# Kernel optimization log

Measured on AMD Instinct MI355X. Metric: run time of the kernel, lower is better.

## Reference

```python
import jax, jax.numpy as jnp
import numpy as np

B, C, S, D = 16, 32, 64, 512
DFF, E = 2048, 8


def setup_inputs() -> dict:
    key = jax.random.key(0)
    ks = jax.random.split(key, 16)
    std = 0.02
    return {
        'x': jax.random.normal(ks[0], (B, C, S, D), jnp.float32),
        'baseline': jax.random.normal(ks[1], (B, C, S, D), jnp.float32),
        'attnres': jax.random.normal(ks[2], (B, C, S, D), jnp.float32),
        'shared_w1': jax.random.normal(ks[3], (DFF, D), jnp.float32) * std,
        'shared_b1': jnp.zeros((DFF,), jnp.float32),
        'shared_w2': jax.random.normal(ks[4], (D, DFF), jnp.float32) * std,
        'shared_b2': jnp.zeros((D,), jnp.float32),
        'spa_router_w': jax.random.normal(ks[5], (E, 3 * D), jnp.float32) * std,
        'spa_router_b': jnp.zeros((E,), jnp.float32),
        'spe_router_w': jax.random.normal(ks[6], (E, 3 * D), jnp.float32) * std,
        'spe_router_b': jnp.zeros((E,), jnp.float32),
        'spa_w1': jax.random.normal(ks[7], (E, DFF, D), jnp.float32) * std,
        'spa_b1': jnp.zeros((E, DFF), jnp.float32),
        'spa_w2': jax.random.normal(ks[8], (E, D, DFF), jnp.float32) * std,
        'spa_b2': jnp.zeros((E, D), jnp.float32),
        'spe_w1': jax.random.normal(ks[9], (E, DFF, D), jnp.float32) * std,
        'spe_b1': jnp.zeros((E, DFF), jnp.float32),
        'spe_w2': jax.random.normal(ks[10], (E, D, DFF), jnp.float32) * std,
        'spe_b2': jnp.zeros((E, D), jnp.float32),
    }


def _route(feat, rw, rb):
    # feat [B, 3D] -> top-1 expert index [B] and its softmax gate weight [B]
    logits = feat @ rw.T + rb            # [B, E]
    p = jax.nn.softmax(logits, axis=-1)
    idx = jnp.argmax(logits, axis=-1)    # [B]
    w = jnp.take_along_axis(p, idx[:, None], axis=-1)[:, 0]
    return idx, w


def _specialist(xf, idx, w1, b1, w2, b2):
    # xf [B, T, D]; per-sample gather of expert weights then batched FFN
    W1, B1 = w1[idx], b1[idx]            # [B, DFF, D], [B, DFF]
    W2, B2 = w2[idx], b2[idx]            # [B, D, DFF], [B, D]
    h = jax.nn.gelu(jnp.einsum('btd,bfd->btf', xf, W1) + B1[:, None, :])
    return jnp.einsum('btf,bdf->btd', h, W2) + B2[:, None, :]


def reference(x, baseline, attnres, shared_w1, shared_b1, shared_w2, shared_b2,
              spa_router_w, spa_router_b, spe_router_w, spe_router_b,
              spa_w1, spa_b1, spa_w2, spa_b2, spe_w1, spe_b1, spe_w2, spe_b2):
    b, d = x.shape[0], x.shape[-1]
    xf = x.reshape(b, -1, d)  # [B, T, D]
    # sample-level AttnRes router features: [B, 3*d_model]
    feat = jnp.concatenate([
        baseline.mean(axis=(1, 2)),
        attnres.mean(axis=(1, 2)),
        (attnres - baseline).mean(axis=(1, 2)),
    ], axis=-1)
    spa_idx, spa_w = _route(feat, spa_router_w, spa_router_b)
    spe_idx, spe_w = _route(feat, spe_router_w, spe_router_b)
    # shared dense FFN (dropout=0 eval)
    shared = jax.nn.gelu(xf @ shared_w1.T + shared_b1) @ shared_w2.T + shared_b2
    spa_out = _specialist(xf, spa_idx, spa_w1, spa_b1, spa_w2, spa_b2)
    spe_out = _specialist(xf, spe_idx, spe_w1, spe_b1, spe_w2, spe_b2)
    y = shared + spa_w[:, None, None] * spa_out + spe_w[:, None, None] * spe_out
    return y.reshape(x.shape)
```

## Files before the change

### kernel.cpp

```cpp
#include <hip/hip_runtime.h>
#include <cstdint>
#include <cstddef>

#define DEV __device__ __forceinline__

typedef unsigned short u16;
typedef _Float16 f16x8 __attribute__((ext_vector_type(8)));
typedef float f32x4 __attribute__((ext_vector_type(4)));

static constexpr int NB  = 16;
static constexpr int T   = 2048;
static constexpr int D   = 512;
static constexpr int DFF = 2048;
static constexpr int NE  = 8;
static constexpr int FEAT = 3 * D;

#define MFMA16 __builtin_amdgcn_mfma_f32_16x16x32_f16

DEV u16 f2h(float f) {
  _Float16 h = (_Float16)f;
  union { _Float16 h; u16 u; } cv; cv.h = h; return cv.u;
}

DEV float gelu_fast(float x) {
  const float t = x * x;
  const float p = x * fmaf(t, -0.07135481627f, -1.59576912161f);
  return __fdividef(x, 1.0f + __expf(p));
}


__global__ void k_part(const float* __restrict__ base, const float* __restrict__ attn,
                       float* __restrict__ part) {
  const int b = blockIdx.x >> 4, ch = blockIdx.x & 15;
  const int d = threadIdx.x;
  const size_t o = ((size_t)b * T + (size_t)ch * 128) * D + d;
  const float* pb = base + o;
  const float* pa = attn + o;
  float sb = 0.f, sa = 0.f;
  for (int r = 0; r < 128; ++r) { sb += pb[(size_t)r * D]; sa += pa[(size_t)r * D]; }
  part[(b * 16 + ch) * D + d] = sb;
  part[NB * 16 * D + (b * 16 + ch) * D + d] = sa;
}

__global__ void k_feat(const float* __restrict__ part, float* __restrict__ feat) {
  const int b = blockIdx.x, d = threadIdx.x;
  float sb = 0.f, sa = 0.f;
  for (int ch = 0; ch < 16; ++ch) {
    sb += part[(b * 16 + ch) * D + d];
    sa += part[NB * 16 * D + (b * 16 + ch) * D + d];
  }
  sb *= (1.0f / 2048.0f); sa *= (1.0f / 2048.0f);
  feat[b * FEAT + d] = sb;
  feat[b * FEAT + D + d] = sa;
  feat[b * FEAT + 2 * D + d] = sa - sb;
}

__global__ void k_zero(int* __restrict__ used) {
  used[threadIdx.x] = 0;
}

__global__ void k_route(const float* __restrict__ feat,
                        const float* __restrict__ rw0, const float* __restrict__ rb0,
                        const float* __restrict__ rw1, const float* __restrict__ rb1,
                        int* __restrict__ idx, float* __restrict__ gate,
                        int* __restrict__ used) {
  const int r = blockIdx.x >> 4, b = blockIdx.x & 15;
  const float* rw = (r == 0) ? rw0 : rw1;
  const float* rb = (r == 0) ? rb0 : rb1;
  const int l = threadIdx.x;
  float p[8];
#pragma unroll
  for (int e = 0; e < 8; ++e) p[e] = 0.f;
  const float* f = feat + b * FEAT;
  for (int k = l; k < FEAT; k += 64) {
    const float fv = f[k];
#pragma unroll
    for (int e = 0; e < 8; ++e) p[e] += fv * rw[e * FEAT + k];
  }
#pragma unroll
  for (int off = 32; off >= 1; off >>= 1) {
#pragma unroll
    for (int e = 0; e < 8; ++e) p[e] += __shfl_xor(p[e], off);
  }
  if (l == 0) {
    float best = -1e30f; int bi = 0;
    float lg[8];
#pragma unroll
    for (int e = 0; e < 8; ++e) {
      lg[e] = p[e] + rb[e];
      if (lg[e] > best) { best = lg[e]; bi = e; }
    }
    float s = 0.f;
#pragma unroll
    for (int e = 0; e < 8; ++e) s += expf(lg[e] - best);
    idx[r * 16 + b] = bi;
    gate[r * 16 + b] = 1.0f / s;
    atomicOr(&used[r * 8 + bi], 1);
  }
}

__global__ void k_btot(const float* __restrict__ b2s, const float* __restrict__ b2a,
                       const float* __restrict__ b2e, const int* __restrict__ idx,
                       const float* __restrict__ gate, float* __restrict__ btot) {
  const int b = blockIdx.x, d = threadIdx.x;
  const int ia = idx[b], ie = idx[16 + b];
  const float ga = gate[b], ge = gate[16 + b];
  btot[b * D + d] = b2s[d] + ga * b2a[ia * D + d] + ge * b2e[ie * D + d];
}

__global__ void k_cast(const float* __restrict__ s, u16* __restrict__ d, long n) {
  const long i = ((long)blockIdx.x * blockDim.x + threadIdx.x) * 4;
  if (i >= n) return;
  const float4 v = *(const float4*)(s + i);
  const unsigned int lo = (unsigned int)f2h(v.x) | ((unsigned int)f2h(v.y) << 16);
  const unsigned int hi = (unsigned int)f2h(v.z) | ((unsigned int)f2h(v.w) << 16);
  *(uint2*)(d + i) = make_uint2(lo, hi);
}

__global__ void k_cast_gated(const float* __restrict__ s, u16* __restrict__ d,
                             const int* __restrict__ used) {
  const int e = blockIdx.x >> 10;
  if (!used[e]) return;
  const long i = (long)e * (DFF * D) + ((long)(blockIdx.x & 1023) * 256 + threadIdx.x) * 4;
  const float4 v = *(const float4*)(s + i);
  const unsigned int lo = (unsigned int)f2h(v.x) | ((unsigned int)f2h(v.y) << 16);
  const unsigned int hi = (unsigned int)f2h(v.z) | ((unsigned int)f2h(v.w) << 16);
  *(uint2*)(d + i) = make_uint2(lo, hi);
}


DEV void ld_lds16(const void* g, void* l) {
  __builtin_amdgcn_global_load_lds((const __attribute__((address_space(1))) void*)g,
                                   (__attribute__((address_space(3))) void*)l, 16, 0, 0);
}

#define BAR __builtin_amdgcn_s_barrier()
#define LGKM0 do { asm volatile("s_waitcnt lgkmcnt(0)" ::: "memory"); \
                   __builtin_amdgcn_sched_barrier(0); } while (0)
#define VMW2 asm volatile("s_waitcnt vmcnt(2)" ::: "memory")
#define VMW0 asm volatile("s_waitcnt vmcnt(0)" ::: "memory")

#define STG_A(tt, h, sb) do { const long ko_ = (long)(tt) * 64;                          \
    ld_lds16(((h) ? gA10 : gA00) + ko_, (char*)As + (sb) * 32768 + (h) * 16384 + dR0);   \
    ld_lds16(((h) ? gA11 : gA01) + ko_, (char*)As + (sb) * 32768 + (h) * 16384 + dR1); } while (0)
#define STG_B(tt, h, sb) do { const long ko_ = (long)(tt) * 64;                          \
    ld_lds16(((h) ? gB10 : gB00) + ko_, (char*)Bs + (sb) * 32768 + (h) * 16384 + dR0);   \
    ld_lds16(((h) ? gB11 : gB01) + ko_, (char*)Bs + (sb) * 32768 + (h) * 16384 + dR1); } while (0)

#define RD_A(dst, mb, sb) do {                                                           \
    _Pragma("unroll") for (int m_ = 0; m_ < 4; ++m_)                                     \
      _Pragma("unroll") for (int k_ = 0; k_ < 2; ++k_)                                   \
        dst[m_][k_] = *(const f16x8*)((const char*)As + (sb) * 32768 + avb[k_] +         \
                                      ((mb) + m_) * 2048); } while (0)
#define RD_B(dst, nb, sb) do {                                                           \
    _Pragma("unroll") for (int n_ = 0; n_ < 2; ++n_)                                     \
      _Pragma("unroll") for (int k_ = 0; k_ < 2; ++k_)                                   \
        dst[n_][k_] = *(const f16x8*)((const char*)Bs + (sb) * 32768 + bvb[k_] +         \
                                      ((nb) + n_) * 2048); } while (0)

#define QUAD(av, bv, mb, nb) do { __builtin_amdgcn_s_setprio(1);                         \
    _Pragma("unroll") for (int m_ = 0; m_ < 4; ++m_)                                     \
      _Pragma("unroll") for (int n_ = 0; n_ < 2; ++n_) {                                 \
        acc[(mb)+m_][(nb)+n_] = MFMA16(av[m_][0], bv[n_][0], acc[(mb)+m_][(nb)+n_],0,0,0); \
        acc[(mb)+m_][(nb)+n_] = MFMA16(av[m_][1], bv[n_][1], acc[(mb)+m_][(nb)+n_],0,0,0); \
      }                                                                                  \
    __builtin_amdgcn_s_setprio(0); } while (0)

#define TILE(tt, sb, STGN, STGA0, VMN) do {                                              \
    RD_A(avLO, 0, sb); RD_B(bvA, 0, sb);                                                 \
    if (STGN) { STG_A((tt)+1, 1, (sb)^1); STG_B((tt)+1, 0, (sb)^1); STG_B((tt)+1, 1, (sb)^1); } \
    BAR; LGKM0; QUAD(avLO, bvA, 0, 0); BAR;                                              \
    RD_B(bvB, 2, sb);                                                                    \
    BAR; LGKM0; QUAD(avLO, bvB, 0, 2); BAR;                                              \
    RD_A(avHI, 4, sb);                                                                   \
    BAR; LGKM0; QUAD(avHI, bvB, 4, 2); BAR;                                              \
    if (STGA0) STG_A((tt)+2, 0, sb);                                                     \
    BAR; __builtin_amdgcn_sched_barrier(0); QUAD(avHI, bvA, 4, 0);                       \
    if ((VMN) == 2) VMW2; else if ((VMN) == 0) VMW0;                                     \
    BAR;                                                                                 \
  } while (0)

template <int NT>
DEV void gemm_8p(const u16* __restrict__ A, int lda, const u16* __restrict__ B, int ldb,
                 u16* As, u16* Bs, f32x4 (&acc)[8][4]) {
  static_assert(NT >= 8 && (NT % 2) == 0, "NT even, >= 8");
  const int tid = threadIdx.x;
  const int lane = tid & 63, wid = tid >> 6;
  const int wr = wid >> 2, wc = wid & 3;

  const int srow = lane >> 3;
  const int scol = (lane & 7) ^ srow;
  const int rj0 = wid * 16 + srow;
  const int rj1 = rj0 + 8;
  const u16* gA00 = A + (size_t)(  0 + rj0) * lda + scol * 8;
  const u16* gA01 = A + (size_t)(  0 + rj1) * lda + scol * 8;
  const u16* gA10 = A + (size_t)(128 + rj0) * lda + scol * 8;
  const u16* gA11 = A + (size_t)(128 + rj1) * lda + scol * 8;
  const u16* gB00 = B + (size_t)(  0 + rj0) * ldb + scol * 8;
  const u16* gB01 = B + (size_t)(  0 + rj1) * ldb + scol * 8;
  const u16* gB10 = B + (size_t)(128 + rj0) * ldb + scol * 8;
  const u16* gB11 = B + (size_t)(128 + rj1) * ldb + scol * 8;
  const int dR0 = (wid * 16) * 128;
  const int dR1 = dR0 + 1024;

  const int aR = wr * 128 + (lane & 15);
  const int bR = wc * 64 + (lane & 15);
  const int sH = lane >> 4;
  int avb[2], bvb[2];
#pragma unroll
  for (int k_ = 0; k_ < 2; ++k_) {
    const int s_ = (k_ * 4 + sH);
    avb[k_] = aR * 128 + ((s_ ^ (lane & 7)) * 16);
    bvb[k_] = bR * 128 + ((s_ ^ (lane & 7)) * 16);
  }

  f16x8 avLO[4][2], avHI[4][2], bvA[2][2], bvB[2][2];

  STG_A(0, 0, 0); STG_A(0, 1, 0); STG_B(0, 0, 0); STG_B(0, 1, 0);
  STG_A(1, 0, 1);
  VMW2; BAR;

  for (int tp = 0; tp < (NT - 2) / 2; ++tp) {
    TILE(2 * tp,     0, true, true, 2);
    TILE(2 * tp + 1, 1, true, true, 2);
  }
  TILE(NT - 2, 0, true,  false, 0);
  TILE(NT - 1, 1, false, false, -1);
}

template <int BANK>
__global__ __launch_bounds__(512) void k_ffn1(
    const u16* __restrict__ xh, const u16* __restrict__ w1, const float* __restrict__ b1,
    const int* __restrict__ idx, const float* __restrict__ gate, u16* __restrict__ h) {
  __shared__ alignas(16) u16 As[2 * 16384];
  __shared__ alignas(16) u16 Bs[2 * 16384];
  int wg = blockIdx.x;
  const int q = (int)gridDim.x >> 3;
  wg = (wg & 7) * q + (wg >> 3);
  const int b  = wg >> 6;
  const int mt = (wg >> 3) & 7;
  const int nt = wg & 7;

  const int e   = (BANK == 0) ? 0 : idx[(BANK - 1) * 16 + b];
  const float g = (BANK == 0) ? 1.0f : gate[(BANK - 1) * 16 + b];
  const u16* Ab = xh + ((size_t)b * T + (size_t)mt * 256) * D;
  const u16* Bb = w1 + (size_t)e * DFF * D + (size_t)nt * 256 * D;
  const float* bb = b1 + (size_t)e * DFF;

  f32x4 acc[8][4];
#pragma unroll
  for (int m = 0; m < 8; ++m)
#pragma unroll
    for (int n = 0; n < 4; ++n)
#pragma unroll
      for (int r = 0; r < 4; ++r) acc[m][n][r] = 0.f;

  gemm_8p<8>(Ab, D, Bb, D, As, Bs, acc);

  const int lane = threadIdx.x & 63, wid = threadIdx.x >> 6;
  const int wr = wid >> 2, wc = wid & 3;
  const int rr = (lane >> 4) << 2, cc = lane & 15;
  const int mrow = mt * 256 + wr * 128;
  const int ncol = nt * 256 + wc * 64;
  u16* hb = h + (size_t)b * T * DFF;
  u16* wsl = (u16*)As + wid * (16 * 72);
  const int rdrow = lane >> 2;
  const int rdcb  = (lane & 3) * 2;
  float bias[4];
#pragma unroll
  for (int n = 0; n < 4; ++n) bias[n] = bb[ncol + n * 16 + cc];
#pragma unroll
  for (int m = 0; m < 8; ++m) {
#pragma unroll
    for (int n = 0; n < 4; ++n) {
      const f32x4 a = acc[m][n];
#pragma unroll
      for (int r = 0; r < 4; ++r)
        wsl[(rr + r) * 72 + n * 16 + cc] = f2h(gelu_fast(a[r] + bias[n]) * g);
    }
    asm volatile("s_waitcnt lgkmcnt(0)" ::: "memory");
    __builtin_amdgcn_sched_barrier(0);
    const uint4 v0 = *(const uint4*)(wsl + rdrow * 72 + rdcb * 8);
    const uint4 v1 = *(const uint4*)(wsl + rdrow * 72 + rdcb * 8 + 8);
    u16* dst = hb + (size_t)(mrow + m * 16 + rdrow) * DFF + ncol + rdcb * 8;
    *(uint4*)dst = v0;
    *(uint4*)(dst + 8) = v1;
    asm volatile("s_waitcnt lgkmcnt(0)" ::: "memory");
    __builtin_amdgcn_sched_barrier(0);
  }
}

template <int BANK>
__global__ __launch_bounds__(512) void k_ffn2(
    const u16* __restrict__ h, const u16* __restrict__ w2, const float* __restrict__ btot,
    const int* __restrict__ idx, float* __restrict__ out) {
  __shared__ alignas(16) u16 As[2 * 16384];
  __shared__ alignas(16) u16 Bs[2 * 16384];
  int wg = blockIdx.x;
  const int q = (int)gridDim.x >> 3;
  wg = (wg & 7) * q + (wg >> 3);
  const int b  = wg >> 4;
  const int mt = (wg >> 1) & 7;
  const int nt = wg & 1;

  const int e = (BANK == 0) ? 0 : idx[(BANK - 1) * 16 + b];
  const u16* Ab = h + ((size_t)b * T + (size_t)mt * 256) * DFF;
  const u16* Bb = w2 + (size_t)e * D * DFF + (size_t)nt * 256 * DFF;

  f32x4 acc[8][4];
#pragma unroll
  for (int m = 0; m < 8; ++m)
#pragma unroll
    for (int n = 0; n < 4; ++n)
#pragma unroll
      for (int r = 0; r < 4; ++r) acc[m][n][r] = 0.f;

  gemm_8p<32>(Ab, DFF, Bb, DFF, As, Bs, acc);

  const int lane = threadIdx.x & 63, wid = threadIdx.x >> 6;
  const int wr = wid >> 2, wc = wid & 3;
  const int rr = (lane >> 4) << 2, cc = lane & 15;
  const int mrow = mt * 256 + wr * 128;
  const int ncol = nt * 256 + wc * 64;
  float* ob = out + (size_t)b * T * D;
  float* wsl = (float*)(void*)As + wid * (16 * 68);
  float btv[4];
#pragma unroll
  for (int n = 0; n < 4; ++n)
    btv[n] = (BANK == 0) ? btot[b * D + ncol + n * 16 + cc] : 0.f;
#pragma unroll
  for (int m = 0; m < 8; ++m) {
#pragma unroll
    for (int n = 0; n < 4; ++n) {
      const f32x4 a = acc[m][n];
#pragma unroll
      for (int r = 0; r < 4; ++r)
        wsl[(rr + r) * 68 + n * 16 + cc] = a[r] + btv[n];
    }
    asm volatile("s_waitcnt lgkmcnt(0)" ::: "memory");
    __builtin_amdgcn_sched_barrier(0);
#pragma unroll
    for (int j = 0; j < 4; ++j) {
      const int row = j * 4 + (lane >> 4);
      const int colb = lane & 15;
      f32x4 v = *(const f32x4*)(wsl + row * 68 + colb * 4);
      float* dst = ob + (size_t)(mrow + m * 16 + row) * D + ncol + colb * 4;
      if (BANK != 0) { const f32x4 o = *(const f32x4*)dst; v += o; }
      *(f32x4*)dst = v;
    }
    asm volatile("s_waitcnt lgkmcnt(0)" ::: "memory");
    __builtin_amdgcn_sched_barrier(0);
  }
}


extern "C" void kernel_launch(void* const* d_in, const int* in_sizes, int n_in,
                              void* d_out, int out_size, void* d_ws, size_t ws_size,
                              hipStream_t stream) {
  (void)in_sizes; (void)n_in; (void)out_size; (void)ws_size;
  const float* x    = (const float*)d_in[0];
  const float* base = (const float*)d_in[1];
  const float* attn = (const float*)d_in[2];
  const float* sw1  = (const float*)d_in[3];
  const float* sb1  = (const float*)d_in[4];
  const float* sw2  = (const float*)d_in[5];
  const float* sb2  = (const float*)d_in[6];
  const float* arw  = (const float*)d_in[7];
  const float* arb  = (const float*)d_in[8];
  const float* erw  = (const float*)d_in[9];
  const float* erb  = (const float*)d_in[10];
  const float* aw1  = (const float*)d_in[11];
  const float* ab1  = (const float*)d_in[12];
  const float* aw2  = (const float*)d_in[13];
  const float* ab2  = (const float*)d_in[14];
  const float* ew1  = (const float*)d_in[15];
  const float* eb1  = (const float*)d_in[16];
  const float* ew2  = (const float*)d_in[17];
  const float* eb2  = (const float*)d_in[18];
  float* out = (float*)d_out;

  char* w = (char*)d_ws;
  u16* xh   = (u16*)w;  w += (size_t)NB * T * D * 2;
  u16* hbuf = (u16*)w;  w += (size_t)NB * T * DFF * 2;
  u16* w1s  = (u16*)w;  w += (size_t)DFF * D * 2;
  u16* w2s  = (u16*)w;  w += (size_t)D * DFF * 2;
  u16* w1a  = (u16*)w;  w += (size_t)NE * DFF * D * 2;
  u16* w2a  = (u16*)w;  w += (size_t)NE * D * DFF * 2;
  u16* w1e  = (u16*)w;  w += (size_t)NE * DFF * D * 2;
  u16* w2e  = (u16*)w;  w += (size_t)NE * D * DFF * 2;
  float* part = (float*)w; w += (size_t)2 * NB * 16 * D * 4;
  float* feat = (float*)w; w += (size_t)NB * FEAT * 4;
  int*   idx  = (int*)w;   w += 32 * 4;
  float* gate = (float*)w; w += 32 * 4;
  float* btot = (float*)w; w += (size_t)NB * D * 4;
  int*   used = (int*)w;   w += 16 * 4;

  k_zero<<<dim3(1), dim3(16), 0, stream>>>(used);
  k_part<<<dim3(256), dim3(512), 0, stream>>>(base, attn, part);
  k_feat<<<dim3(16), dim3(512), 0, stream>>>(part, feat);
  k_route<<<dim3(32), dim3(64), 0, stream>>>(feat, arw, arb, erw, erb, idx, gate, used);
  k_btot<<<dim3(16), dim3(512), 0, stream>>>(sb2, ab2, eb2, idx, gate, btot);

  {
    long n;
    n = (long)NB * T * D;  k_cast<<<(unsigned)(n / 1024), 256, 0, stream>>>(x,   xh,  n);
    n = (long)DFF * D;     k_cast<<<(unsigned)(n / 1024), 256, 0, stream>>>(sw1, w1s, n);
    n = (long)D * DFF;     k_cast<<<(unsigned)(n / 1024), 256, 0, stream>>>(sw2, w2s, n);
    k_cast_gated<<<dim3(8192), 256, 0, stream>>>(aw1, w1a, used);
    k_cast_gated<<<dim3(8192), 256, 0, stream>>>(aw2, w2a, used);
    k_cast_gated<<<dim3(8192), 256, 0, stream>>>(ew1, w1e, used + 8);
    k_cast_gated<<<dim3(8192), 256, 0, stream>>>(ew2, w2e, used + 8);
  }

  const dim3 g1(1024), g2(256), blk(512);
  k_ffn1<0><<<g1, blk, 0, stream>>>(xh, w1s, sb1, idx, gate, hbuf);
  k_ffn2<0><<<g2, blk, 0, stream>>>(hbuf, w2s, btot, idx, out);
  k_ffn1<1><<<g1, blk, 0, stream>>>(xh, w1a, ab1, idx, gate, hbuf);
  k_ffn2<1><<<g2, blk, 0, stream>>>(hbuf, w2a, btot, idx, out);
  k_ffn1<2><<<g1, blk, 0, stream>>>(xh, w1e, eb1, idx, gate, hbuf);
  k_ffn2<2><<<g2, blk, 0, stream>>>(hbuf, w2e, btot, idx, out);
}
```

Measured before the change: 719.1 us.

## Make FFN1 blocks persistent over four M tiles and merge cast launches

The first FFN GEMM now launches 256 workgroups instead of 1024. Each workgroup walks four consecutive 256-row M tiles as one continuous 32-step K pipeline and runs the GELU epilogue for each finished tile while loads for the next tile are already in flight. A separate LDS scratch buffer is added for the epilogue so it does not clash with the staging buffers. The seven cast launches are merged into two kernels to cut launch overhead. The trade-offs are extra LDS use and fewer workgroups per GPU, which may lower occupancy and load balance.

```diff
diff --git a/kernel.cpp b/kernel.cpp
--- a/kernel.cpp
+++ b/kernel.cpp
@@ -108,24 +108,37 @@
   btot[b * D + d] = b2s[d] + ga * b2a[ia * D + d] + ge * b2e[ie * D + d];
 }
 
-__global__ void k_cast(const float* __restrict__ s, u16* __restrict__ d, long n) {
-  const long i = ((long)blockIdx.x * blockDim.x + threadIdx.x) * 4;
-  if (i >= n) return;
+
+DEV void cast4(const float* __restrict__ s, u16* __restrict__ d, long i) {
   const float4 v = *(const float4*)(s + i);
   const unsigned int lo = (unsigned int)f2h(v.x) | ((unsigned int)f2h(v.y) << 16);
   const unsigned int hi = (unsigned int)f2h(v.z) | ((unsigned int)f2h(v.w) << 16);
   *(uint2*)(d + i) = make_uint2(lo, hi);
 }
 
-__global__ void k_cast_gated(const float* __restrict__ s, u16* __restrict__ d,
-                             const int* __restrict__ used) {
-  const int e = blockIdx.x >> 10;
-  if (!used[e]) return;
+__global__ void k_cast3(const float* __restrict__ x, const float* __restrict__ sw1,
+                        const float* __restrict__ sw2, u16* __restrict__ xh,
+                        u16* __restrict__ w1s, u16* __restrict__ w2s) {
+  const long NX = (long)NB * T * D;
+  const long NW = (long)DFF * D;
+  const long t = ((long)blockIdx.x * 256 + threadIdx.x) * 4;
+  if (t < NX)               cast4(x,   xh,  t);
+  else if (t < NX + NW)     cast4(sw1, w1s, t - NX);
+  else                      cast4(sw2, w2s, t - NX - NW);
+}
+
+__global__ void k_castg(const float* __restrict__ aw1, const float* __restrict__ aw2,
+                        const float* __restrict__ ew1, const float* __restrict__ ew2,
+                        u16* __restrict__ w1a, u16* __restrict__ w2a,
+                        u16* __restrict__ w1e, u16* __restrict__ w2e,
+                        const int* __restrict__ used) {
+  const int rg = blockIdx.x >> 13;
+  const int e  = (blockIdx.x >> 10) & 7;
+  if (!used[(rg >= 2 ? 8 : 0) + e]) return;
   const long i = (long)e * (DFF * D) + ((long)(blockIdx.x & 1023) * 256 + threadIdx.x) * 4;
-  const float4 v = *(const float4*)(s + i);
-  const unsigned int lo = (unsigned int)f2h(v.x) | ((unsigned int)f2h(v.y) << 16);
-  const unsigned int hi = (unsigned int)f2h(v.z) | ((unsigned int)f2h(v.w) << 16);
-  *(uint2*)(d + i) = make_uint2(lo, hi);
+  const float* s = (rg == 0) ? aw1 : (rg == 1) ? aw2 : (rg == 2) ? ew1 : ew2;
+  u16*         d = (rg == 0) ? w1a : (rg == 1) ? w2a : (rg == 2) ? w1e : w2e;
+  cast4(s, d, i);
 }
 
 
@@ -139,13 +152,6 @@
                    __builtin_amdgcn_sched_barrier(0); } while (0)
 #define VMW2 asm volatile("s_waitcnt vmcnt(2)" ::: "memory")
 #define VMW0 asm volatile("s_waitcnt vmcnt(0)" ::: "memory")
-
-#define STG_A(tt, h, sb) do { const long ko_ = (long)(tt) * 64;                          \
-    ld_lds16(((h) ? gA10 : gA00) + ko_, (char*)As + (sb) * 32768 + (h) * 16384 + dR0);   \
-    ld_lds16(((h) ? gA11 : gA01) + ko_, (char*)As + (sb) * 32768 + (h) * 16384 + dR1); } while (0)
-#define STG_B(tt, h, sb) do { const long ko_ = (long)(tt) * 64;                          \
-    ld_lds16(((h) ? gB10 : gB00) + ko_, (char*)Bs + (sb) * 32768 + (h) * 16384 + dR0);   \
-    ld_lds16(((h) ? gB11 : gB01) + ko_, (char*)Bs + (sb) * 32768 + (h) * 16384 + dR1); } while (0)
 
 #define RD_A(dst, mb, sb) do {                                                           \
     _Pragma("unroll") for (int m_ = 0; m_ < 4; ++m_)                                     \
@@ -165,6 +171,39 @@
         acc[(mb)+m_][(nb)+n_] = MFMA16(av[m_][1], bv[n_][1], acc[(mb)+m_][(nb)+n_],0,0,0); \
       }                                                                                  \
     __builtin_amdgcn_s_setprio(0); } while (0)
+
+#define CORE_SETUP(Abase, Bbase, lda, ldb)                                               \
+  const int srow = lane >> 3;                                                            \
+  const int scol = (lane & 7) ^ srow;                                                    \
+  const int rj0 = wid * 16 + srow;                                                       \
+  const int rj1 = rj0 + 8;                                                               \
+  const u16* gA00 = (Abase) + (size_t)(  0 + rj0) * (lda) + scol * 8;                    \
+  const u16* gA01 = (Abase) + (size_t)(  0 + rj1) * (lda) + scol * 8;                    \
+  const u16* gA10 = (Abase) + (size_t)(128 + rj0) * (lda) + scol * 8;                    \
+  const u16* gA11 = (Abase) + (size_t)(128 + rj1) * (lda) + scol * 8;                    \
+  const u16* gB00 = (Bbase) + (size_t)(  0 + rj0) * (ldb) + scol * 8;                    \
+  const u16* gB01 = (Bbase) + (size_t)(  0 + rj1) * (ldb) + scol * 8;                    \
+  const u16* gB10 = (Bbase) + (size_t)(128 + rj0) * (ldb) + scol * 8;                    \
+  const u16* gB11 = (Bbase) + (size_t)(128 + rj1) * (ldb) + scol * 8;                    \
+  const int dR0 = (wid * 16) * 128;                                                      \
+  const int dR1 = dR0 + 1024;                                                            \
+  const int aR = wr * 128 + (lane & 15);                                                 \
+  const int bR = wc * 64 + (lane & 15);                                                  \
+  const int sH = lane >> 4;                                                              \
+  int avb[2], bvb[2];                                                                    \
+  _Pragma("unroll") for (int k_ = 0; k_ < 2; ++k_) {                                     \
+    const int s_ = (k_ * 4 + sH);                                                        \
+    avb[k_] = aR * 128 + ((s_ ^ (lane & 7)) * 16);                                       \
+    bvb[k_] = bR * 128 + ((s_ ^ (lane & 7)) * 16);                                       \
+  }
+
+
+#define STG_A(tt, h, sb) do { const long ko_ = (long)(tt) * 64;                          \
+    ld_lds16(((h) ? gA10 : gA00) + ko_, (char*)As + (sb) * 32768 + (h) * 16384 + dR0);   \
+    ld_lds16(((h) ? gA11 : gA01) + ko_, (char*)As + (sb) * 32768 + (h) * 16384 + dR1); } while (0)
+#define STG_B(tt, h, sb) do { const long ko_ = (long)(tt) * 64;                          \
+    ld_lds16(((h) ? gB10 : gB00) + ko_, (char*)Bs + (sb) * 32768 + (h) * 16384 + dR0);   \
+    ld_lds16(((h) ? gB11 : gB01) + ko_, (char*)Bs + (sb) * 32768 + (h) * 16384 + dR1); } while (0)
 
 #define TILE(tt, sb, STGN, STGA0, VMN) do {                                              \
     RD_A(avLO, 0, sb); RD_B(bvA, 0, sb);                                                 \
@@ -180,53 +219,28 @@
     BAR;                                                                                 \
   } while (0)
 
-template <int NT>
-DEV void gemm_8p(const u16* __restrict__ A, int lda, const u16* __restrict__ B, int ldb,
-                 u16* As, u16* Bs, f32x4 (&acc)[8][4]) {
-  static_assert(NT >= 8 && (NT % 2) == 0, "NT even, >= 8");
-  const int tid = threadIdx.x;
-  const int lane = tid & 63, wid = tid >> 6;
-  const int wr = wid >> 2, wc = wid & 3;
-
-  const int srow = lane >> 3;
-  const int scol = (lane & 7) ^ srow;
-  const int rj0 = wid * 16 + srow;
-  const int rj1 = rj0 + 8;
-  const u16* gA00 = A + (size_t)(  0 + rj0) * lda + scol * 8;
-  const u16* gA01 = A + (size_t)(  0 + rj1) * lda + scol * 8;
-  const u16* gA10 = A + (size_t)(128 + rj0) * lda + scol * 8;
-  const u16* gA11 = A + (size_t)(128 + rj1) * lda + scol * 8;
-  const u16* gB00 = B + (size_t)(  0 + rj0) * ldb + scol * 8;
-  const u16* gB01 = B + (size_t)(  0 + rj1) * ldb + scol * 8;
-  const u16* gB10 = B + (size_t)(128 + rj0) * ldb + scol * 8;
-  const u16* gB11 = B + (size_t)(128 + rj1) * ldb + scol * 8;
-  const int dR0 = (wid * 16) * 128;
-  const int dR1 = dR0 + 1024;
-
-  const int aR = wr * 128 + (lane & 15);
-  const int bR = wc * 64 + (lane & 15);
-  const int sH = lane >> 4;
-  int avb[2], bvb[2];
-#pragma unroll
-  for (int k_ = 0; k_ < 2; ++k_) {
-    const int s_ = (k_ * 4 + sH);
-    avb[k_] = aR * 128 + ((s_ ^ (lane & 7)) * 16);
-    bvb[k_] = bR * 128 + ((s_ ^ (lane & 7)) * 16);
-  }
-
-  f16x8 avLO[4][2], avHI[4][2], bvA[2][2], bvB[2][2];
-
-  STG_A(0, 0, 0); STG_A(0, 1, 0); STG_B(0, 0, 0); STG_B(0, 1, 0);
-  STG_A(1, 0, 1);
-  VMW2; BAR;
-
-  for (int tp = 0; tp < (NT - 2) / 2; ++tp) {
-    TILE(2 * tp,     0, true, true, 2);
-    TILE(2 * tp + 1, 1, true, true, 2);
-  }
-  TILE(NT - 2, 0, true,  false, 0);
-  TILE(NT - 1, 1, false, false, -1);
-}
+
+#define STG_A1(tt, h, sb) do {                                                           \
+    const long o_ = (long)((tt) >> 3) * (256L * D) + (long)((tt) & 7) * 64;              \
+    ld_lds16(((h) ? gA10 : gA00) + o_, (char*)As + (sb) * 32768 + (h) * 16384 + dR0);    \
+    ld_lds16(((h) ? gA11 : gA01) + o_, (char*)As + (sb) * 32768 + (h) * 16384 + dR1); } while (0)
+#define STG_B1(tt, h, sb) do { const long o_ = (long)((tt) & 7) * 64;                    \
+    ld_lds16(((h) ? gB10 : gB00) + o_, (char*)Bs + (sb) * 32768 + (h) * 16384 + dR0);    \
+    ld_lds16(((h) ? gB11 : gB01) + o_, (char*)Bs + (sb) * 32768 + (h) * 16384 + dR1); } while (0)
+
+#define TILE1(tt, sb, STGN, STGA0, VMN) do {                                             \
+    RD_A(avLO, 0, sb); RD_B(bvA, 0, sb);                                                 \
+    if (STGN) { STG_A1((tt)+1, 1, (sb)^1); STG_B1((tt)+1, 0, (sb)^1); STG_B1((tt)+1, 1, (sb)^1); } \
+    BAR; LGKM0; QUAD(avLO, bvA, 0, 0); BAR;                                              \
+    RD_B(bvB, 2, sb);                                                                    \
+    BAR; LGKM0; QUAD(avLO, bvB, 0, 2); BAR;                                              \
+    RD_A(avHI, 4, sb);                                                                   \
+    BAR; LGKM0; QUAD(avHI, bvB, 4, 2); BAR;                                              \
+    if (STGA0) STG_A1((tt)+2, 0, sb);                                                    \
+    BAR; __builtin_amdgcn_sched_barrier(0); QUAD(avHI, bvA, 4, 0);                       \
+    if ((VMN) == 2) VMW2; else if ((VMN) == 0) VMW0;                                     \
+    BAR;                                                                                 \
+  } while (0)
 
 template <int BANK>
 __global__ __launch_bounds__(512) void k_ffn1(
@@ -234,19 +248,25 @@
     const int* __restrict__ idx, const float* __restrict__ gate, u16* __restrict__ h) {
   __shared__ alignas(16) u16 As[2 * 16384];
   __shared__ alignas(16) u16 Bs[2 * 16384];
+  __shared__ alignas(16) u16 eps[8 * 16 * 72];
   int wg = blockIdx.x;
   const int q = (int)gridDim.x >> 3;
   wg = (wg & 7) * q + (wg >> 3);
-  const int b  = wg >> 6;
-  const int mt = (wg >> 3) & 7;
-  const int nt = wg & 7;
+  const int b   = wg >> 4;
+  const int nt  = (wg >> 1) & 7;
+  const int mtg = wg & 1;
 
   const int e   = (BANK == 0) ? 0 : idx[(BANK - 1) * 16 + b];
   const float g = (BANK == 0) ? 1.0f : gate[(BANK - 1) * 16 + b];
-  const u16* Ab = xh + ((size_t)b * T + (size_t)mt * 256) * D;
+  const u16* Ab = xh + ((size_t)b * T + (size_t)mtg * 1024) * D;
   const u16* Bb = w1 + (size_t)e * DFF * D + (size_t)nt * 256 * D;
   const float* bb = b1 + (size_t)e * DFF;
 
+  const int tid = threadIdx.x;
+  const int lane = tid & 63, wid = tid >> 6;
+  const int wr = wid >> 2, wc = wid & 3;
+  CORE_SETUP(Ab, Bb, D, D)
+
   f32x4 acc[8][4];
 #pragma unroll
   for (int m = 0; m < 8; ++m)
@@ -255,39 +275,56 @@
 #pragma unroll
       for (int r = 0; r < 4; ++r) acc[m][n][r] = 0.f;
 
-  gemm_8p<8>(Ab, D, Bb, D, As, Bs, acc);
-
-  const int lane = threadIdx.x & 63, wid = threadIdx.x >> 6;
-  const int wr = wid >> 2, wc = wid & 3;
-  const int rr = (lane >> 4) << 2, cc = lane & 15;
-  const int mrow = mt * 256 + wr * 128;
+  f16x8 avLO[4][2], avHI[4][2], bvA[2][2], bvB[2][2];
+
+  const int rrE = (lane >> 4) << 2, ccE = lane & 15;
   const int ncol = nt * 256 + wc * 64;
   u16* hb = h + (size_t)b * T * DFF;
-  u16* wsl = (u16*)As + wid * (16 * 72);
+  u16* wslE = eps + wid * (16 * 72);
   const int rdrow = lane >> 2;
   const int rdcb  = (lane & 3) * 2;
   float bias[4];
 #pragma unroll
-  for (int n = 0; n < 4; ++n) bias[n] = bb[ncol + n * 16 + cc];
-#pragma unroll
-  for (int m = 0; m < 8; ++m) {
-#pragma unroll
-    for (int n = 0; n < 4; ++n) {
-      const f32x4 a = acc[m][n];
-#pragma unroll
-      for (int r = 0; r < 4; ++r)
-        wsl[(rr + r) * 72 + n * 16 + cc] = f2h(gelu_fast(a[r] + bias[n]) * g);
+  for (int n = 0; n < 4; ++n) bias[n] = bb[ncol + n * 16 + ccE];
+
+  auto epi = [&](int s) {
+    const int mrow = mtg * 1024 + s * 256 + wr * 128;
+#pragma unroll
+    for (int m = 0; m < 8; ++m) {
+#pragma unroll
+      for (int n = 0; n < 4; ++n) {
+        const f32x4 a = acc[m][n];
+#pragma unroll
+        for (int r = 0; r < 4; ++r)
+          wslE[(rrE + r) * 72 + n * 16 + ccE] = f2h(gelu_fast(a[r] + bias[n]) * g);
+        acc[m][n][0] = 0.f; acc[m][n][1] = 0.f; acc[m][n][2] = 0.f; acc[m][n][3] = 0.f;
+      }
+      asm volatile("s_waitcnt lgkmcnt(0)" ::: "memory");
+      __builtin_amdgcn_sched_barrier(0);
+      const uint4 v0 = *(const uint4*)(wslE + rdrow * 72 + rdcb * 8);
+      const uint4 v1 = *(const uint4*)(wslE + rdrow * 72 + rdcb * 8 + 8);
+      u16* dst = hb + (size_t)(mrow + m * 16 + rdrow) * DFF + ncol + rdcb * 8;
+      *(uint4*)dst = v0;
+      *(uint4*)(dst + 8) = v1;
+      asm volatile("s_waitcnt lgkmcnt(0)" ::: "memory");
+      __builtin_amdgcn_sched_barrier(0);
     }
-    asm volatile("s_waitcnt lgkmcnt(0)" ::: "memory");
-    __builtin_amdgcn_sched_barrier(0);
-    const uint4 v0 = *(const uint4*)(wsl + rdrow * 72 + rdcb * 8);
-    const uint4 v1 = *(const uint4*)(wsl + rdrow * 72 + rdcb * 8 + 8);
-    u16* dst = hb + (size_t)(mrow + m * 16 + rdrow) * DFF + ncol + rdcb * 8;
-    *(uint4*)dst = v0;
-    *(uint4*)(dst + 8) = v1;
-    asm volatile("s_waitcnt lgkmcnt(0)" ::: "memory");
-    __builtin_amdgcn_sched_barrier(0);
-  }
+  };
+
+  STG_A1(0, 0, 0); STG_A1(0, 1, 0); STG_B1(0, 0, 0); STG_B1(0, 1, 0);
+  STG_A1(1, 0, 1);
+  VMW2; BAR;
+
+  for (int tp = 0; tp < 15; ++tp) {
+    TILE1(2 * tp,     0, true, true, 2);
+    TILE1(2 * tp + 1, 1, true, true, 2);
+    if (tp == 3) epi(0);
+    else if (tp == 7) epi(1);
+    else if (tp == 11) epi(2);
+  }
+  TILE1(30, 0, true,  false, 0);
+  TILE1(31, 1, false, false, -1);
+  epi(3);
 }
 
 template <int BANK>
@@ -307,6 +344,11 @@
   const u16* Ab = h + ((size_t)b * T + (size_t)mt * 256) * DFF;
   const u16* Bb = w2 + (size_t)e * D * DFF + (size_t)nt * 256 * DFF;
 
+  const int tid = threadIdx.x;
+  const int lane = tid & 63, wid = tid >> 6;
+  const int wr = wid >> 2, wc = wid & 3;
+  CORE_SETUP(Ab, Bb, DFF, DFF)
+
   f32x4 acc[8][4];
 #pragma unroll
   for (int m = 0; m < 8; ++m)
@@ -315,10 +357,18 @@
 #pragma unroll
       for (int r = 0; r < 4; ++r) acc[m][n][r] = 0.f;
 
-  gemm_8p<32>(Ab, DFF, Bb, DFF, As, Bs, acc);
-
-  const int lane = threadIdx.x & 63, wid = threadIdx.x >> 6;
-  const int wr = wid >> 2, wc = wid & 3;
+  f16x8 avLO[4][2], avHI[4][2], bvA[2][2], bvB[2][2];
+
+  STG_A(0, 0, 0); STG_A(0, 1, 0); STG_B(0, 0, 0); STG_B(0, 1, 0);
+  STG_A(1, 0, 1);
+  VMW2; BAR;
+  for (int tp = 0; tp < 15; ++tp) {
+    TILE(2 * tp,     0, true, true, 2);
+    TILE(2 * tp + 1, 1, true, true, 2);
+  }
+  TILE(30, 0, true,  false, 0);
+  TILE(31, 1, false, false, -1);
+
   const int rr = (lane >> 4) << 2, cc = lane & 15;
   const int mrow = mt * 256 + wr * 128;
   const int ncol = nt * 256 + wc * 64;
@@ -401,18 +451,10 @@
   k_route<<<dim3(32), dim3(64), 0, stream>>>(feat, arw, arb, erw, erb, idx, gate, used);
   k_btot<<<dim3(16), dim3(512), 0, stream>>>(sb2, ab2, eb2, idx, gate, btot);
 
-  {
-    long n;
-    n = (long)NB * T * D;  k_cast<<<(unsigned)(n / 1024), 256, 0, stream>>>(x,   xh,  n);
-    n = (long)DFF * D;     k_cast<<<(unsigned)(n / 1024), 256, 0, stream>>>(sw1, w1s, n);
-    n = (long)D * DFF;     k_cast<<<(unsigned)(n / 1024), 256, 0, stream>>>(sw2, w2s, n);
-    k_cast_gated<<<dim3(8192), 256, 0, stream>>>(aw1, w1a, used);
-    k_cast_gated<<<dim3(8192), 256, 0, stream>>>(aw2, w2a, used);
-    k_cast_gated<<<dim3(8192), 256, 0, stream>>>(ew1, w1e, used + 8);
-    k_cast_gated<<<dim3(8192), 256, 0, stream>>>(ew2, w2e, used + 8);
-  }
-
-  const dim3 g1(1024), g2(256), blk(512);
+  k_cast3<<<dim3(18432), 256, 0, stream>>>(x, sw1, sw2, xh, w1s, w2s);
+  k_castg<<<dim3(32768), 256, 0, stream>>>(aw1, aw2, ew1, ew2, w1a, w2a, w1e, w2e, used);
+
+  const dim3 g1(256), g2(256), blk(512);
   k_ffn1<0><<<g1, blk, 0, stream>>>(xh, w1s, sb1, idx, gate, hbuf);
   k_ffn2<0><<<g2, blk, 0, stream>>>(hbuf, w2s, btot, idx, out);
   k_ffn1<1><<<g1, blk, 0, stream>>>(xh, w1a, ab1, idx, gate, hbuf);
```

Measured after the change: 997.8 us. 38.8% more time.

## Merge cast kernels and make FFN1 blocks compute two M-tiles each

Applied to the files above, without the earlier changes.

The seven fp32-to-fp16 cast launches are merged into two kernels: one for x and the shared weights, one gated kernel covering all four expert weight banks. The FFN1 grid is halved to 512 workgroups, and each workgroup now runs two sequential passes over adjacent 256-row M tiles while reusing the same weight column tile. The epilogue staging buffer moves into the upper half of Bs so it stays clear of A staging. The aim is to cut launch overhead and spread fixed per-block costs over more work. The risk is less parallelism in FFN1, with only 512 blocks, and possible LDS reuse hazards between the epilogue and the next pass's GEMM staging.

```diff
diff --git a/kernel.cpp b/kernel.cpp
--- a/kernel.cpp
+++ b/kernel.cpp
@@ -108,24 +108,37 @@
   btot[b * D + d] = b2s[d] + ga * b2a[ia * D + d] + ge * b2e[ie * D + d];
 }
 
-__global__ void k_cast(const float* __restrict__ s, u16* __restrict__ d, long n) {
-  const long i = ((long)blockIdx.x * blockDim.x + threadIdx.x) * 4;
-  if (i >= n) return;
+
+DEV void cast4(const float* __restrict__ s, u16* __restrict__ d, long i) {
   const float4 v = *(const float4*)(s + i);
   const unsigned int lo = (unsigned int)f2h(v.x) | ((unsigned int)f2h(v.y) << 16);
   const unsigned int hi = (unsigned int)f2h(v.z) | ((unsigned int)f2h(v.w) << 16);
   *(uint2*)(d + i) = make_uint2(lo, hi);
 }
 
-__global__ void k_cast_gated(const float* __restrict__ s, u16* __restrict__ d,
-                             const int* __restrict__ used) {
-  const int e = blockIdx.x >> 10;
-  if (!used[e]) return;
+__global__ void k_cast3(const float* __restrict__ x, const float* __restrict__ sw1,
+                        const float* __restrict__ sw2, u16* __restrict__ xh,
+                        u16* __restrict__ w1s, u16* __restrict__ w2s) {
+  const long NX = (long)NB * T * D;
+  const long NW = (long)DFF * D;
+  const long t = ((long)blockIdx.x * 256 + threadIdx.x) * 4;
+  if (t < NX)               cast4(x,   xh,  t);
+  else if (t < NX + NW)     cast4(sw1, w1s, t - NX);
+  else                      cast4(sw2, w2s, t - NX - NW);
+}
+
+__global__ void k_castg(const float* __restrict__ aw1, const float* __restrict__ aw2,
+                        const float* __restrict__ ew1, const float* __restrict__ ew2,
+                        u16* __restrict__ w1a, u16* __restrict__ w2a,
+                        u16* __restrict__ w1e, u16* __restrict__ w2e,
+                        const int* __restrict__ used) {
+  const int rg = blockIdx.x >> 13;
+  const int e  = (blockIdx.x >> 10) & 7;
+  if (!used[(rg >= 2 ? 8 : 0) + e]) return;
   const long i = (long)e * (DFF * D) + ((long)(blockIdx.x & 1023) * 256 + threadIdx.x) * 4;
-  const float4 v = *(const float4*)(s + i);
-  const unsigned int lo = (unsigned int)f2h(v.x) | ((unsigned int)f2h(v.y) << 16);
-  const unsigned int hi = (unsigned int)f2h(v.z) | ((unsigned int)f2h(v.w) << 16);
-  *(uint2*)(d + i) = make_uint2(lo, hi);
+  const float* s = (rg == 0) ? aw1 : (rg == 1) ? aw2 : (rg == 2) ? ew1 : ew2;
+  u16*         d = (rg == 0) ? w1a : (rg == 1) ? w2a : (rg == 2) ? w1e : w2e;
+  cast4(s, d, i);
 }
 
 
@@ -237,56 +250,62 @@
   int wg = blockIdx.x;
   const int q = (int)gridDim.x >> 3;
   wg = (wg & 7) * q + (wg >> 3);
-  const int b  = wg >> 6;
-  const int mt = (wg >> 3) & 7;
-  const int nt = wg & 7;
+  const int b   = wg >> 5;
+  const int mtp = (wg >> 3) & 3;
+  const int nt  = wg & 7;
 
   const int e   = (BANK == 0) ? 0 : idx[(BANK - 1) * 16 + b];
   const float g = (BANK == 0) ? 1.0f : gate[(BANK - 1) * 16 + b];
-  const u16* Ab = xh + ((size_t)b * T + (size_t)mt * 256) * D;
   const u16* Bb = w1 + (size_t)e * DFF * D + (size_t)nt * 256 * D;
   const float* bb = b1 + (size_t)e * DFF;
-
-  f32x4 acc[8][4];
-#pragma unroll
-  for (int m = 0; m < 8; ++m)
-#pragma unroll
-    for (int n = 0; n < 4; ++n)
-#pragma unroll
-      for (int r = 0; r < 4; ++r) acc[m][n][r] = 0.f;
-
-  gemm_8p<8>(Ab, D, Bb, D, As, Bs, acc);
 
   const int lane = threadIdx.x & 63, wid = threadIdx.x >> 6;
   const int wr = wid >> 2, wc = wid & 3;
   const int rr = (lane >> 4) << 2, cc = lane & 15;
-  const int mrow = mt * 256 + wr * 128;
   const int ncol = nt * 256 + wc * 64;
   u16* hb = h + (size_t)b * T * DFF;
-  u16* wsl = (u16*)As + wid * (16 * 72);
+  u16* wslE = (u16*)Bs + 16384 + wid * 1152;
   const int rdrow = lane >> 2;
   const int rdcb  = (lane & 3) * 2;
   float bias[4];
 #pragma unroll
   for (int n = 0; n < 4; ++n) bias[n] = bb[ncol + n * 16 + cc];
-#pragma unroll
-  for (int m = 0; m < 8; ++m) {
-#pragma unroll
-    for (int n = 0; n < 4; ++n) {
-      const f32x4 a = acc[m][n];
-#pragma unroll
-      for (int r = 0; r < 4; ++r)
-        wsl[(rr + r) * 72 + n * 16 + cc] = f2h(gelu_fast(a[r] + bias[n]) * g);
+
+  f32x4 acc[8][4];
+
+#pragma unroll 1
+  for (int pass = 0; pass < 2; ++pass) {
+#pragma unroll
+    for (int m = 0; m < 8; ++m)
+#pragma unroll
+      for (int n = 0; n < 4; ++n)
+#pragma unroll
+        for (int r = 0; r < 4; ++r) acc[m][n][r] = 0.f;
+
+    const int mtl = mtp * 2 + pass;
+    const u16* Ab = xh + ((size_t)b * T + (size_t)mtl * 256) * D;
+    gemm_8p<8>(Ab, D, Bb, D, As, Bs, acc);
+
+    const int mrow = mtl * 256 + wr * 128;
+#pragma unroll
+    for (int m = 0; m < 8; ++m) {
+#pragma unroll
+      for (int n = 0; n < 4; ++n) {
+        const f32x4 a = acc[m][n];
+#pragma unroll
+        for (int r = 0; r < 4; ++r)
+          wslE[(rr + r) * 72 + n * 16 + cc] = f2h(gelu_fast(a[r] + bias[n]) * g);
+      }
+      asm volatile("s_waitcnt lgkmcnt(0)" ::: "memory");
+      __builtin_amdgcn_sched_barrier(0);
+      const uint4 v0 = *(const uint4*)(wslE + rdrow * 72 + rdcb * 8);
+      const uint4 v1 = *(const uint4*)(wslE + rdrow * 72 + rdcb * 8 + 8);
+      u16* dst = hb + (size_t)(mrow + m * 16 + rdrow) * DFF + ncol + rdcb * 8;
+      *(uint4*)dst = v0;
+      *(uint4*)(dst + 8) = v1;
+      asm volatile("s_waitcnt lgkmcnt(0)" ::: "memory");
+      __builtin_amdgcn_sched_barrier(0);
     }
-    asm volatile("s_waitcnt lgkmcnt(0)" ::: "memory");
-    __builtin_amdgcn_sched_barrier(0);
-    const uint4 v0 = *(const uint4*)(wsl + rdrow * 72 + rdcb * 8);
-    const uint4 v1 = *(const uint4*)(wsl + rdrow * 72 + rdcb * 8 + 8);
-    u16* dst = hb + (size_t)(mrow + m * 16 + rdrow) * DFF + ncol + rdcb * 8;
-    *(uint4*)dst = v0;
-    *(uint4*)(dst + 8) = v1;
-    asm volatile("s_waitcnt lgkmcnt(0)" ::: "memory");
-    __builtin_amdgcn_sched_barrier(0);
   }
 }
 
@@ -401,18 +420,10 @@
   k_route<<<dim3(32), dim3(64), 0, stream>>>(feat, arw, arb, erw, erb, idx, gate, used);
   k_btot<<<dim3(16), dim3(512), 0, stream>>>(sb2, ab2, eb2, idx, gate, btot);
 
-  {
-    long n;
-    n = (long)NB * T * D;  k_cast<<<(unsigned)(n / 1024), 256, 0, stream>>>(x,   xh,  n);
-    n = (long)DFF * D;     k_cast<<<(unsigned)(n / 1024), 256, 0, stream>>>(sw1, w1s, n);
-    n = (long)D * DFF;     k_cast<<<(unsigned)(n / 1024), 256, 0, stream>>>(sw2, w2s, n);
-    k_cast_gated<<<dim3(8192), 256, 0, stream>>>(aw1, w1a, used);
-    k_cast_gated<<<dim3(8192), 256, 0, stream>>>(aw2, w2a, used);
-    k_cast_gated<<<dim3(8192), 256, 0, stream>>>(ew1, w1e, used + 8);
-    k_cast_gated<<<dim3(8192), 256, 0, stream>>>(ew2, w2e, used + 8);
-  }
-
-  const dim3 g1(1024), g2(256), blk(512);
+  k_cast3<<<dim3(18432), 256, 0, stream>>>(x, sw1, sw2, xh, w1s, w2s);
+  k_castg<<<dim3(32768), 256, 0, stream>>>(aw1, aw2, ew1, ew2, w1a, w2a, w1e, w2e, used);
+
+  const dim3 g1(512), g2(256), blk(512);
   k_ffn1<0><<<g1, blk, 0, stream>>>(xh, w1s, sb1, idx, gate, hbuf);
   k_ffn2<0><<<g2, blk, 0, stream>>>(hbuf, w2s, btot, idx, out);
   k_ffn1<1><<<g1, blk, 0, stream>>>(xh, w1a, ab1, idx, gate, hbuf);
```

Result: slower. 908.8 us (+26.4%).
